# Optimization experiments

Measured on AMD Instinct MI355X. Metric: run time of the kernel, lower is better.

The kernel has to match this reference:

```python
import jax, jax.numpy as jnp
import numpy as np

KH, KW, STRIDE, PAD, DIL = 3, 3, 1, 1, 1


def setup_inputs() -> dict:
    key = jax.random.key(0)
    ks = jax.random.split(key, 4)
    B, C, H, W, O = 4, 256, 64, 64, 256
    K = KH * KW
    x = jax.random.normal(ks[0], (B, C, H, W), jnp.float32)
    # offset/mask conv params (original inits to zero; use small random so offsets are non-trivial)
    w_om = jax.random.normal(ks[1], (3 * K, C, KH, KW), jnp.float32) * 0.01
    b_om = jnp.zeros((3 * K,), jnp.float32)
    # main weight: kaiming_uniform_(a=1) -> gain = sqrt(2/(1+1^2)) = 1, bound = sqrt(3)/sqrt(fan_in)
    fan_in = C * K
    bound = float(np.sqrt(3.0) / np.sqrt(fan_in))
    weight = jax.random.uniform(ks[2], (O, C, KH, KW), jnp.float32, -bound, bound)
    bias = jnp.zeros((O,), jnp.float32)
    return {"x": x, "w_om": w_om, "b_om": b_om, "weight": weight, "bias": bias}


def _deform_conv2d(x, offset, mask, weight, bias):
    # torchvision.ops.deform_conv2d semantics, deformable_groups=1, stride=1, pad=1, dil=1
    B, C, H, W = x.shape
    K = KH * KW
    # torchvision offset layout: per-tap interleaved (y, x) pairs along channel dim
    off_y = offset[:, 0::2]  # [B, K, H, W]
    off_x = offset[:, 1::2]  # [B, K, H, W]
    ky = (jnp.repeat(jnp.arange(KH), KW) * DIL).astype(x.dtype)  # [K]
    kx = (jnp.tile(jnp.arange(KW), KH) * DIL).astype(x.dtype)    # [K]
    base_y = (jnp.arange(H) * STRIDE - PAD).astype(x.dtype)
    base_x = (jnp.arange(W) * STRIDE - PAD).astype(x.dtype)
    py = base_y[None, None, :, None] + ky[None, :, None, None] + off_y  # [B,K,H,W]
    px = base_x[None, None, None, :] + kx[None, :, None, None] + off_x  # [B,K,H,W]
    y0 = jnp.floor(py)
    x0 = jnp.floor(px)
    ly = py - y0
    lx = px - x0
    y0i = y0.astype(jnp.int32)
    x0i = x0.astype(jnp.int32)
    x_flat = x.reshape(B, C, H * W)

    def gather(yy, xx):
        # zero-padded gather of one bilinear corner -> [B, C, K, H, W]
        valid = ((yy >= 0) & (yy < H) & (xx >= 0) & (xx < W)).astype(x.dtype)
        idx = (jnp.clip(yy, 0, H - 1) * W + jnp.clip(xx, 0, W - 1)).reshape(B, -1)
        g = jax.vmap(lambda xf, i: jnp.take(xf, i, axis=1))(x_flat, idx)
        return g.reshape(B, C, K, H, W) * valid.reshape(B, 1, K, H, W)

    w00 = ((1 - ly) * (1 - lx))[:, None]
    w01 = ((1 - ly) * lx)[:, None]
    w10 = (ly * (1 - lx))[:, None]
    w11 = (ly * lx)[:, None]
    val = (gather(y0i, x0i) * w00 + gather(y0i, x0i + 1) * w01
           + gather(y0i + 1, x0i) * w10 + gather(y0i + 1, x0i + 1) * w11)
    cols = val * mask[:, None]  # modulated columns [B,C,K,H,W]
    out = jnp.einsum('bckhw,ock->bohw', cols, weight.reshape(weight.shape[0], C, K))
    return out + bias[None, :, None, None]


def reference(x, w_om, b_om, weight, bias):
    om = jax.lax.conv_general_dilated(
        x, w_om, (STRIDE, STRIDE), ((PAD, PAD), (PAD, PAD)),
        rhs_dilation=(DIL, DIL), dimension_numbers=('NCHW', 'OIHW', 'NCHW'),
    ) + b_om[None, :, None, None]
    K = KH * KW
    o1, o2, m = om[:, :K], om[:, K:2 * K], om[:, 2 * K:]
    offset = jnp.concatenate([o1, o2], axis=1)  # [B, 2K, H, W]
    mask = jax.nn.sigmoid(m)                    # [B, K, H, W]
    return _deform_conv2d(x, offset, mask, weight, bias)
```

## Files before the change

### kernel.cpp

```cpp
#include <hip/hip_runtime.h>
#include <stdint.h>

#define B_ 4
#define C_ 256
#define H_ 64
#define W_ 64
#define O_ 256
#define K_ 9
#define CK 2304
#define HW 4096
#define NTOT 16384

typedef __bf16 bf16x8 __attribute__((ext_vector_type(8)));
typedef __bf16 bf16x4 __attribute__((ext_vector_type(4)));
typedef float f32x4 __attribute__((ext_vector_type(4)));
typedef float f32x2 __attribute__((ext_vector_type(2)));
typedef f32x2 __attribute__((aligned(4))) f32x2u;

__device__ __forceinline__ uint16_t f2bf(float f) {
  uint32_t u = __builtin_bit_cast(uint32_t, f);
  return (uint16_t)((u + 0x7FFFu + ((u >> 16) & 1u)) >> 16);
}

__device__ __forceinline__ uint32_t pk_bf16(float a, float b) {
  uint16_t lo = __builtin_bit_cast(uint16_t, (__bf16)a);
  uint16_t hi = __builtin_bit_cast(uint16_t, (__bf16)b);
  return (uint32_t)lo | ((uint32_t)hi << 16);
}

__global__ void kA_prep(const float* __restrict__ weight, const float* __restrict__ w_om,
                        const float* __restrict__ x, uint16_t* __restrict__ wb,
                        uint16_t* __restrict__ womb, uint16_t* __restrict__ xT) {
  int bx = blockIdx.x;
  int t = threadIdx.x;
  if (bx < 256) {
    int o = bx, c = t;
    const float* wp = weight + (o * 256 + c) * 9;
#pragma unroll
    for (int k = 0; k < 9; ++k) wb[o * CK + k * 256 + c] = f2bf(wp[k]);
  } else if (bx < 283) {
    int j = bx - 256, c = t;
    const float* wp = w_om + (j * 256 + c) * 9;
#pragma unroll
    for (int k = 0; k < 9; ++k) womb[j * CK + k * 256 + c] = f2bf(wp[k]);
  } else if (bx < 288) {
    int j = 27 + (bx - 283), c = t;
#pragma unroll
    for (int k = 0; k < 9; ++k) womb[j * CK + k * 256 + c] = 0;
  } else {
    int bxl = bx - 288;
    int ct = bxl & 3;
    int hwt = (bxl >> 2) & 63;
    int b = bxl >> 8;
    int l = t & 63;
    int cq = t >> 6;

    __shared__ __align__(16) uint16_t tile[64 * 72];

    const float* xb = x + ((b * 256 + ct * 64) * HW) + hwt * 64;
#pragma unroll
    for (int i = 0; i < 16; ++i) {
      int c = cq * 16 + i;
      tile[l * 72 + c] = f2bf(xb[c * HW + l]);
    }
    __syncthreads();

    int hw = t >> 2;
    int c8 = (t & 3) * 8;
    uint16_t* dst = xT + ((size_t)b << 20) + (size_t)(hwt * 64 + hw) * 256 + ct * 64;
    *(uint4*)&dst[c8] = *(const uint4*)&tile[hw * 72 + c8];
    *(uint4*)&dst[c8 + 32] = *(const uint4*)&tile[hw * 72 + c8 + 32];
  }
}


struct GatherState {
  float wa0[4], wb0[4], wa1[4], wb1[4];
  bf16x4 r00[4], r01[4], r10[4], r11[4];
};

__device__ __forceinline__ void gather_issue(GatherState& S, const uint16_t* __restrict__ xb,
                                             const float* pypx_l,
                                             int kg, int rbase, int lane) {
#pragma unroll
  for (int j = 0; j < 4; ++j) {
    int nrow = rbase + j;
    float py = pypx_l[(0 * 9 + kg) * 64 + nrow];
    float px = pypx_l[(1 * 9 + kg) * 64 + nrow];
    float mk = pypx_l[(2 * 9 + kg) * 64 + nrow];
    float fy0 = floorf(py), fx0 = floorf(px);
    float ly = py - fy0, lx = px - fx0;
    int y0 = (int)fy0, x0 = (int)fx0;
    bool vy0 = ((unsigned)y0 < 64u), vy1 = ((unsigned)(y0 + 1) < 64u);
    bool vx0 = ((unsigned)x0 < 64u), vx1 = ((unsigned)(x0 + 1) < 64u);
    float w00 = (vy0 && vx0) ? (1.f - ly) * (1.f - lx) * mk : 0.f;
    float w01 = (vy0 && vx1) ? (1.f - ly) * lx * mk : 0.f;
    float w10 = (vy1 && vx0) ? ly * (1.f - lx) * mk : 0.f;
    float w11 = (vy1 && vx1) ? ly * lx * mk : 0.f;
    bool sel0 = (x0 >= 63);
    bool sel1 = (x0 >= 0);
    S.wa0[j] = (sel0 ? 0.f : w00) + (sel1 ? 0.f : w01);
    S.wb0[j] = (sel0 ? w00 : 0.f) + (sel1 ? w01 : 0.f);
    S.wa1[j] = (sel0 ? 0.f : w10) + (sel1 ? 0.f : w11);
    S.wb1[j] = (sel0 ? w10 : 0.f) + (sel1 ? w11 : 0.f);
    int bx0 = min(max(x0, 0), 62);
    int a0 = min(max(y0, 0), 63) * 64 + bx0;
    int a1 = min(max(y0 + 1, 0), 63) * 64 + bx0;
    S.r00[j] = *(const bf16x4*)&xb[a0 * 256 + lane * 4];
    S.r01[j] = *(const bf16x4*)&xb[a0 * 256 + 256 + lane * 4];
    S.r10[j] = *(const bf16x4*)&xb[a1 * 256 + lane * 4];
    S.r11[j] = *(const bf16x4*)&xb[a1 * 256 + 256 + lane * 4];
  }
}

__device__ __forceinline__ void gather_finish(const GatherState& S, uint16_t* bslab,
                                              int rbase, int lane) {
#pragma unroll
  for (int j = 0; j < 4; ++j) {
    int nrow = rbase + j;
    float v[4];
#pragma unroll
    for (int i = 0; i < 4; ++i)
      v[i] = S.wa0[j] * (float)S.r00[j][i] + S.wb0[j] * (float)S.r01[j][i] +
             S.wa1[j] * (float)S.r10[j][i] + S.wb1[j] * (float)S.r11[j][i];
    uint2 pk;
    pk.x = pk_bf16(v[0], v[1]);
    pk.y = pk_bf16(v[2], v[3]);
    int chunk = lane >> 1;
    int chs = (chunk & 24) | ((chunk & 7) ^ (nrow & 7));
    *(uint2*)&bslab[nrow * 256 + chs * 8 + (lane & 1) * 4] = pk;
  }
}

__device__ __forceinline__ void stageA(const uint16_t* __restrict__ wb, uint16_t* asbuf,
                                       int kbase, int t) {
#pragma unroll
  for (int i = 0; i < 4; ++i) {
    int rr = i * 64 + (t >> 3);
    const uint16_t* src = wb + rr * CK + kbase + (((t & 7) ^ (rr & 7)) << 3);
    __builtin_amdgcn_global_load_lds(
        (const __attribute__((address_space(1))) uint32_t*)src,
        (__attribute__((address_space(3))) uint32_t*)&asbuf[i * 4096 + t * 8], 16, 0, 0);
  }
}

__device__ __forceinline__ void mma_step(const uint16_t* AsP, const uint16_t* BsP,
                                         f32x4 acc[4][2], int wm, int wn, int lr, int q,
                                         int kt2) {
#pragma unroll
  for (int kc = 0; kc < 2; ++kc) {
    bf16x8 aF[4], bF[2];
#pragma unroll
    for (int i = 0; i < 4; ++i) {
      int row = wm * 64 + i * 16 + lr;
      aF[i] = *(const bf16x8*)&AsP[row * 64 + (((kc * 4 + q) ^ (row & 7)) << 3)];
    }
#pragma unroll
    for (int j = 0; j < 2; ++j) {
      int row = wn * 32 + j * 16 + lr;
      int kidx = kt2 * 8 + kc * 4 + q;
      int chs = (kidx & 24) | ((kidx & 7) ^ (row & 7));
      bF[j] = *(const bf16x8*)&BsP[row * 256 + chs * 8];
    }
#pragma unroll
    for (int i = 0; i < 4; ++i)
#pragma unroll
      for (int j = 0; j < 2; ++j)
        acc[i][j] = __builtin_amdgcn_mfma_f32_16x16x32_bf16(aF[i], bF[j], acc[i][j], 0, 0, 0);
  }
}

__global__ __launch_bounds__(512, 2) void k123(const uint16_t* __restrict__ wb,
                                               const uint16_t* __restrict__ womb,
                                               const uint16_t* __restrict__ xT,
                                               const float* __restrict__ b_om,
                                               const float* __restrict__ bias,
                                               float* __restrict__ out) {
  __shared__ __align__(16) uint16_t As[2][16384];
  __shared__ __align__(16) uint16_t Bs[16384];
  __shared__ float pypx_l[3 * 9 * 64];

  int t = threadIdx.x;
  int lane = t & 63;
  int wid = __builtin_amdgcn_readfirstlane(t >> 6);
  int lr = lane & 15, q = lane >> 4;
  int bx = blockIdx.x;
  int swz = (bx & 7) * 32 + (bx >> 3);
  int n0 = swz * 64;
  int b = n0 >> 12;
  int hw0 = n0 & 4095;
  const uint16_t* xb = xT + ((size_t)b << 20);

  {
    int ns4 = wid & 3;
    int kh2 = wid >> 2;
    int hw = (n0 + ns4 * 16 + lr) & 4095;
    int y = hw >> 6, xx = hw & 63;
    const uint16_t* zrow = womb + 31 * CK;

    f32x4 acc0 = {0.f, 0.f, 0.f, 0.f};
    f32x4 acc1 = {0.f, 0.f, 0.f, 0.f};

    int ks = kh2 ? 4 : 0;
    int ke = kh2 ? 9 : 4;
    for (int k = ks; k < ke; ++k) {
      int dy = k / 3, dx = k - dy * 3;
      int ny = y + dy - 1, nx = xx + dx - 1;
      bool valid = ((unsigned)ny < 64u) && ((unsigned)nx < 64u);
      int row = (min(max(ny, 0), 63) << 6) + min(max(nx, 0), 63);
      const uint16_t* bp = valid ? (xb + row * 256 + q * 8) : (zrow + q * 8);
      const uint16_t* ap = womb + lr * CK + k * 256 + q * 8;
#pragma unroll
      for (int kt = 0; kt < 8; ++kt) {
        int c0 = kt * 32;
        bf16x8 bF = *(const bf16x8*)&bp[c0];
        bf16x8 aF0 = *(const bf16x8*)&ap[c0];
        bf16x8 aF1 = *(const bf16x8*)&ap[16 * CK + c0];
        acc0 = __builtin_amdgcn_mfma_f32_16x16x32_bf16(aF0, bF, acc0, 0, 0, 0);
        acc1 = __builtin_amdgcn_mfma_f32_16x16x32_bf16(aF1, bF, acc1, 0, 0, 0);
      }
    }

    float* red = (float*)As;
    int base = ((kh2 * 4 + ns4) * 64 + lane) * 8;
#pragma unroll
    for (int r = 0; r < 4; ++r) {
      red[base + r] = acc0[r];
      red[base + 4 + r] = acc1[r];
    }
    __syncthreads();

    if (kh2 == 0) {
      int b0 = (ns4 * 64 + lane) * 8;
      int b1 = ((4 + ns4) * 64 + lane) * 8;
      int nn = ns4 * 16 + lr;
#pragma unroll
      for (int i = 0; i < 8; ++i) {
        float s = red[b0 + i] + red[b1 + i];
        int j = (i < 4) ? (q * 4 + i) : (16 + q * 4 + (i - 4));
        if (j < 27) {
          float v = s + b_om[j];
          if (j < 18) {
            int k = j >> 1;
            if ((j & 1) == 0)
              pypx_l[(0 * 9 + k) * 64 + nn] = (float)(y - 1 + k / 3) + v;
            else
              pypx_l[(1 * 9 + k) * 64 + nn] = (float)(xx - 1 + k % 3) + v;
          } else {
            pypx_l[(2 * 9 + (j - 18)) * 64 + nn] = 1.f / (1.f + __expf(-v));
          }
        }
      }
    }
    __syncthreads();
  }

  f32x4 acc[4][2];
  const f32x4 zero = {0.f, 0.f, 0.f, 0.f};
#pragma unroll
  for (int i = 0; i < 4; ++i)
#pragma unroll
    for (int j = 0; j < 2; ++j) acc[i][j] = zero;

  int wm = wid >> 1, wn = wid & 1;
  GatherState S;
  int wrow = wid * 8;

  gather_issue(S, xb, pypx_l, 0, wrow, lane);
  gather_finish(S, Bs, wrow, lane);
  gather_issue(S, xb, pypx_l, 0, wrow + 4, lane);
  gather_finish(S, Bs, wrow + 4, lane);
  stageA(wb, As[0], 0, t);
  __syncthreads();

  for (int k = 0; k < 9; ++k) {
    for (int kt2 = 0; kt2 < 4; ++kt2) {
      if (!(k == 8 && kt2 == 3)) {
        int kb2 = (kt2 == 3) ? (k + 1) * 256 : k * 256 + (kt2 + 1) * 64;
        stageA(wb, As[(kt2 + 1) & 1], kb2, t);
      }
      mma_step(As[kt2 & 1], Bs, acc, wm, wn, lr, q, kt2);
      __syncthreads();
    }
    if (k < 8) {
      gather_issue(S, xb, pypx_l, k + 1, wrow, lane);
      gather_finish(S, Bs, wrow, lane);
      gather_issue(S, xb, pypx_l, k + 1, wrow + 4, lane);
      gather_finish(S, Bs, wrow + 4, lane);
      __syncthreads();
    }
  }

#pragma unroll
  for (int i = 0; i < 4; ++i) {
#pragma unroll
    for (int r = 0; r < 4; ++r) {
      int o = wm * 64 + i * 16 + q * 4 + r;
      float bv = bias[o];
      float* orow = out + (b * O_ + o) * HW + hw0;
#pragma unroll
      for (int j = 0; j < 2; ++j) orow[wn * 32 + j * 16 + lr] = acc[i][j][r] + bv;
    }
  }
}

__global__ void k0_wconv(const float* __restrict__ weight, uint16_t* __restrict__ wb) {
  int idx = blockIdx.x * 256 + threadIdx.x;
  if (idx >= O_ * CK) return;
  int o = idx / CK;
  int rem = idx - o * CK;
  int k = rem >> 8;
  int c = rem & 255;
  wb[idx] = f2bf(weight[(o * C_ + c) * K_ + k]);
}

__global__ void k1_offconv(const float* __restrict__ x, const float* __restrict__ w_om,
                           const float* __restrict__ b_om, float* __restrict__ pypxmk) {
  int bx = blockIdx.x;
  int jq = bx % 7;
  int h = (bx / 7) % H_;
  int b = bx / (7 * H_);
  int t = threadIdx.x;
  int w = t & 63;
  int cs = __builtin_amdgcn_readfirstlane(t >> 6);

  float acc[4] = {0.f, 0.f, 0.f, 0.f};
  const float* xb = x + (b * C_) * HW;

  for (int ci = 0; ci < 64; ++ci) {
    int c = cs * 64 + ci;
    const float* xr = xb + c * HW;
    float xv[3][3];
#pragma unroll
    for (int r = 0; r < 3; ++r) {
      int y = h - 1 + r;
      bool yv = ((unsigned)y < 64u);
#pragma unroll
      for (int dx = 0; dx < 3; ++dx) {
        int xx = w - 1 + dx;
        bool v = yv && ((unsigned)xx < 64u);
        xv[r][dx] = v ? xr[y * 64 + xx] : 0.f;
      }
    }
    const float* wp = w_om + ((jq * 4) * C_ + c) * 9;
#pragma unroll
    for (int jj = 0; jj < 4; ++jj) {
      int j = jq * 4 + jj;
      int jeff = (j < 27) ? jj : 0;
      const float* wj = wp + jeff * (C_ * 9);
      float a = 0.f;
#pragma unroll
      for (int r = 0; r < 3; ++r)
#pragma unroll
        for (int dx = 0; dx < 3; ++dx)
          a = fmaf(xv[r][dx], wj[r * 3 + dx], a);
      acc[jj] += a;
    }
  }

  __shared__ float red[4][4][64];
#pragma unroll
  for (int jj = 0; jj < 4; ++jj) red[cs][jj][w] = acc[jj];
  __syncthreads();

  int jj = t >> 6;
  int j = jq * 4 + jj;
  if (j < 27) {
    float s = red[0][jj][w] + red[1][jj][w] + red[2][jj][w] + red[3][jj][w] + b_om[j];
    float* pyA = pypxmk;
    float* pxA = pypxmk + 147456;
    float* mkA = pypxmk + 294912;
    if (j < 18) {
      int k = j >> 1;
      int off = (b * 9 + k) * HW + h * 64 + w;
      if ((j & 1) == 0)
        pyA[off] = (float)(h - 1 + k / 3) + s;
      else
        pxA[off] = (float)(w - 1 + k % 3) + s;
    } else {
      int k = j - 18;
      mkA[(b * 9 + k) * HW + h * 64 + w] = 1.f / (1.f + __expf(-s));
    }
  }
}

__global__ void k2_fb(const float* __restrict__ x, const float* __restrict__ pypxmk,
                      uint16_t* __restrict__ cols) {
  int bx = blockIdx.x;
  int cg2 = bx & 15;
  int h = (bx >> 4) & 63;
  int b = bx >> 10;
  int t = threadIdx.x;
  int w = t & 63;
  int g = t >> 6;

  const float* pyA = pypxmk;
  const float* pxA = pypxmk + 147456;
  const float* mkA = pypxmk + 294912;

  __shared__ uint16_t tile[64 * 146];
  const float* xb = x + b * C_ * HW;
  int cbase = cg2 * 16 + g * 4;

#pragma unroll
  for (int k = 0; k < 9; ++k) {
    int poff = (b * 9 + k) * HW + h * 64 + w;
    float py = pyA[poff];
    float px = pxA[poff];
    float mk = mkA[poff];
    float fy0 = floorf(py), fx0 = floorf(px);
    float ly = py - fy0, lx = px - fx0;
    int y0 = (int)fy0, x0 = (int)fx0;
    bool vy0 = ((unsigned)y0 < 64u), vy1 = ((unsigned)(y0 + 1) < 64u);
    bool vx0 = ((unsigned)x0 < 64u), vx1 = ((unsigned)(x0 + 1) < 64u);
    float w00 = (vy0 && vx0) ? (1.f - ly) * (1.f - lx) * mk : 0.f;
    float w01 = (vy0 && vx1) ? (1.f - ly) * lx * mk : 0.f;
    float w10 = (vy1 && vx0) ? ly * (1.f - lx) * mk : 0.f;
    float w11 = (vy1 && vx1) ? ly * lx * mk : 0.f;
    bool sel0 = (x0 >= 63);
    bool sel1 = (x0 >= 0);
    float wa0 = (sel0 ? 0.f : w00) + (sel1 ? 0.f : w01);
    float wb0 = (sel0 ? w00 : 0.f) + (sel1 ? w01 : 0.f);
    float wa1 = (sel0 ? 0.f : w10) + (sel1 ? 0.f : w11);
    float wb1 = (sel0 ? w10 : 0.f) + (sel1 ? w11 : 0.f);
    int bx0 = min(max(x0, 0), 62);
    int a0 = min(max(y0, 0), 63) * 64 + bx0;
    int a1 = min(max(y0 + 1, 0), 63) * 64 + bx0;

#pragma unroll
    for (int cp = 0; cp < 2; ++cp) {
      const float* xcA = xb + (cbase + cp * 2) * HW;
      const float* xcB = xcA + HW;
      f32x2 A0 = *(const f32x2u*)&xcA[a0];
      f32x2 A1 = *(const f32x2u*)&xcA[a1];
      f32x2 B0 = *(const f32x2u*)&xcB[a0];
      f32x2 B1 = *(const f32x2u*)&xcB[a1];
      float rA = wa0 * A0.x + wb0 * A0.y + wa1 * A1.x + wb1 * A1.y;
      float rB = wa0 * B0.x + wb0 * B0.y + wa1 * B1.x + wb1 * B1.y;
      *(uint32_t*)&tile[w * 146 + k * 16 + g * 4 + cp * 2] = pk_bf16(rA, rB);
    }
  }
  __syncthreads();

#pragma unroll
  for (int it = 0; it < 18; ++it) {
    int u = t + it * 256;
    int wu = u / 72;
    int rem = u - wu * 72;
    int k = rem >> 3;
    int cd = rem & 7;
    uint32_t val = *(const uint32_t*)&tile[wu * 146 + rem * 2];
    int n = b * HW + h * 64 + wu;
    int dst = n * CK + k * 256 + cg2 * 16 + cd * 2;
    *(uint32_t*)&cols[dst] = val;
  }
}

__global__ void k3_flex(const uint16_t* __restrict__ wb, const uint16_t* __restrict__ cols,
                        const float* __restrict__ bias, float* __restrict__ out) {
  int bx = blockIdx.x;
  int mt = bx & 1;
  int nt = bx >> 1;
  int o0 = mt * 128;
  int n0 = nt * 128;
  int t = threadIdx.x;
  int lane = t & 63;
  int wid = t >> 6;
  int wm = wid >> 1, wn = wid & 1;
  int lr = lane & 15, q = lane >> 4;

  __shared__ __align__(16) uint16_t As[128 * 32];
  __shared__ __align__(16) uint16_t Bs[128 * 32];

  f32x4 acc[4][4];
  const f32x4 zero = {0.f, 0.f, 0.f, 0.f};
#pragma unroll
  for (int i = 0; i < 4; ++i)
#pragma unroll
    for (int j = 0; j < 4; ++j) acc[i][j] = zero;

  int r0 = t >> 2;
  int koff = (t & 3) * 8;
  const uint16_t* gA = wb + (o0 + r0) * CK + koff;
  const uint16_t* gB = cols + (n0 + r0) * CK + koff;

  for (int kt = 0; kt < 72; ++kt) {
    int k0 = kt * 32;
    __builtin_amdgcn_global_load_lds(
        (const __attribute__((address_space(1))) uint32_t*)(gA + k0),
        (__attribute__((address_space(3))) uint32_t*)&As[t * 8], 16, 0, 0);
    __builtin_amdgcn_global_load_lds(
        (const __attribute__((address_space(1))) uint32_t*)(gA + 64 * CK + k0),
        (__attribute__((address_space(3))) uint32_t*)&As[2048 + t * 8], 16, 0, 0);
    __builtin_amdgcn_global_load_lds(
        (const __attribute__((address_space(1))) uint32_t*)(gB + k0),
        (__attribute__((address_space(3))) uint32_t*)&Bs[t * 8], 16, 0, 0);
    __builtin_amdgcn_global_load_lds(
        (const __attribute__((address_space(1))) uint32_t*)(gB + 64 * CK + k0),
        (__attribute__((address_space(3))) uint32_t*)&Bs[2048 + t * 8], 16, 0, 0);
    __syncthreads();

    bf16x8 aF[4], bF[4];
#pragma unroll
    for (int i = 0; i < 4; ++i)
      aF[i] = *(const bf16x8*)&As[(wm * 64 + i * 16 + lr) * 32 + q * 8];
#pragma unroll
    for (int j = 0; j < 4; ++j)
      bF[j] = *(const bf16x8*)&Bs[(wn * 64 + j * 16 + lr) * 32 + q * 8];
#pragma unroll
    for (int i = 0; i < 4; ++i)
#pragma unroll
      for (int j = 0; j < 4; ++j)
        acc[i][j] = __builtin_amdgcn_mfma_f32_16x16x32_bf16(aF[i], bF[j], acc[i][j], 0, 0, 0);
    __syncthreads();
  }

  int bb = n0 >> 12;
  int hw0 = n0 & 4095;
#pragma unroll
  for (int i = 0; i < 4; ++i) {
#pragma unroll
    for (int r = 0; r < 4; ++r) {
      int o = o0 + wm * 64 + i * 16 + q * 4 + r;
      float bv = bias[o];
      float* orow = out + (bb * O_ + o) * HW + hw0;
#pragma unroll
      for (int j = 0; j < 4; ++j) orow[wn * 64 + j * 16 + lr] = acc[i][j][r] + bv;
    }
  }
}

extern "C" void kernel_launch(void* const* d_in, const int* in_sizes, int n_in,
                              void* d_out, int out_size, void* d_ws, size_t ws_size,
                              hipStream_t stream) {
  const float* x = (const float*)d_in[0];
  const float* w_om = (const float*)d_in[1];
  const float* b_om = (const float*)d_in[2];
  const float* weight = (const float*)d_in[3];
  const float* bias = (const float*)d_in[4];
  float* out = (float*)d_out;

  char* ws = (char*)d_ws;
  uint16_t* wb = (uint16_t*)ws;
  uint16_t* womb = (uint16_t*)(ws + 1179648);
  uint16_t* xT = (uint16_t*)(ws + 1327104);

  if (ws_size >= 11485184ull) {
    hipLaunchKernelGGL(kA_prep, dim3(1312), dim3(256), 0, stream, weight, w_om, x, wb, womb, xT);
    hipLaunchKernelGGL(k123, dim3(256), dim3(512), 0, stream, wb, womb, xT, b_om, bias, out);
  } else {
    float* pypx_fb = (float*)(ws + 1179648);
    uint16_t* colsf = (uint16_t*)(ws + 2949120);
    hipLaunchKernelGGL(k0_wconv, dim3(2304), dim3(256), 0, stream, weight, wb);
    hipLaunchKernelGGL(k1_offconv, dim3(4 * 64 * 7), dim3(256), 0, stream, x, w_om, b_om, pypx_fb);
    hipLaunchKernelGGL(k2_fb, dim3(4 * 64 * 16), dim3(256), 0, stream, x, pypx_fb, colsf);
    hipLaunchKernelGGL(k3_flex, dim3(256), dim3(256), 0, stream, wb, colsf, bias, out);
  }
}
```

Before: 158.7 us.

## Stage offset-conv prologue operands in LDS via async global_load_lds

```diff
diff --git a/kernel.cpp b/kernel.cpp
--- a/kernel.cpp
+++ b/kernel.cpp
@@ -192,63 +192,69 @@
   const uint16_t* xb = xT + ((size_t)b << 20);
 
   {
-    int ns4 = wid & 3;
-    int kh2 = wid >> 2;
-    int hw = (n0 + ns4 * 16 + lr) & 4095;
-    int y = hw >> 6, xx = hw & 63;
+    uint16_t* Apro = As[0];
+    int jh = wid >> 2, ng = wid & 3;
     const uint16_t* zrow = womb + 31 * CK;
-
-    f32x4 acc0 = {0.f, 0.f, 0.f, 0.f};
-    f32x4 acc1 = {0.f, 0.f, 0.f, 0.f};
-
-    int ks = kh2 ? 4 : 0;
-    int ke = kh2 ? 9 : 4;
-    for (int k = ks; k < ke; ++k) {
-      int dy = k / 3, dx = k - dy * 3;
-      int ny = y + dy - 1, nx = xx + dx - 1;
-      bool valid = ((unsigned)ny < 64u) && ((unsigned)nx < 64u);
-      int row = (min(max(ny, 0), 63) << 6) + min(max(nx, 0), 63);
-      const uint16_t* bp = valid ? (xb + row * 256 + q * 8) : (zrow + q * 8);
-      const uint16_t* ap = womb + lr * CK + k * 256 + q * 8;
+    f32x4 accp = {0.f, 0.f, 0.f, 0.f};
+
+    for (int k = 0; k < 9; ++k) {
+      int dy = k / 3 - 1, dx = k - (k / 3) * 3 - 1;
+#pragma unroll
+      for (int i = 0; i < 2; ++i) {
+        int id = i * 512 + t;
+        int row = id >> 5, c5 = id & 31;
+        int cs = (c5 & 24) | ((c5 & 7) ^ (row & 7));
+        const uint16_t* src = womb + row * CK + k * 256 + cs * 8;
+        __builtin_amdgcn_global_load_lds(
+            (const __attribute__((address_space(1))) uint32_t*)src,
+            (__attribute__((address_space(3))) uint32_t*)&Apro[row * 256 + c5 * 8], 16, 0, 0);
+      }
+#pragma unroll
+      for (int i = 0; i < 4; ++i) {
+        int id = i * 512 + t;
+        int nrow = id >> 5, c5 = id & 31;
+        int hw = (n0 + nrow) & 4095;
+        int y = hw >> 6, xx = hw & 63;
+        int ny = y + dy, nx = xx + dx;
+        bool valid = ((unsigned)ny < 64u) && ((unsigned)nx < 64u);
+        int row_g = (ny << 6) + nx;
+        int cs = (c5 & 24) | ((c5 & 7) ^ (nrow & 7));
+        const uint16_t* src = valid ? (xb + row_g * 256 + cs * 8) : (zrow + cs * 8);
+        __builtin_amdgcn_global_load_lds(
+            (const __attribute__((address_space(1))) uint32_t*)src,
+            (__attribute__((address_space(3))) uint32_t*)&Bs[nrow * 256 + c5 * 8], 16, 0, 0);
+      }
+      __syncthreads();
 #pragma unroll
       for (int kt = 0; kt < 8; ++kt) {
-        int c0 = kt * 32;
-        bf16x8 bF = *(const bf16x8*)&bp[c0];
-        bf16x8 aF0 = *(const bf16x8*)&ap[c0];
-        bf16x8 aF1 = *(const bf16x8*)&ap[16 * CK + c0];
-        acc0 = __builtin_amdgcn_mfma_f32_16x16x32_bf16(aF0, bF, acc0, 0, 0, 0);
-        acc1 = __builtin_amdgcn_mfma_f32_16x16x32_bf16(aF1, bF, acc1, 0, 0, 0);
+        int kidx = kt * 4 + q;
+        int arow = jh * 16 + lr;
+        int achs = (kidx & 24) | ((kidx & 7) ^ (arow & 7));
+        bf16x8 aF = *(const bf16x8*)&Apro[arow * 256 + achs * 8];
+        int brow = ng * 16 + lr;
+        int bchs = (kidx & 24) | ((kidx & 7) ^ (brow & 7));
+        bf16x8 bF = *(const bf16x8*)&Bs[brow * 256 + bchs * 8];
+        accp = __builtin_amdgcn_mfma_f32_16x16x32_bf16(aF, bF, accp, 0, 0, 0);
       }
-    }
-
-    float* red = (float*)As;
-    int base = ((kh2 * 4 + ns4) * 64 + lane) * 8;
+      __syncthreads();
+    }
+
+    int nn = ng * 16 + lr;
+    int hwp = (n0 + nn) & 4095;
+    int yp = hwp >> 6, xp = hwp & 63;
 #pragma unroll
     for (int r = 0; r < 4; ++r) {
-      red[base + r] = acc0[r];
-      red[base + 4 + r] = acc1[r];
-    }
-    __syncthreads();
-
-    if (kh2 == 0) {
-      int b0 = (ns4 * 64 + lane) * 8;
-      int b1 = ((4 + ns4) * 64 + lane) * 8;
-      int nn = ns4 * 16 + lr;
-#pragma unroll
-      for (int i = 0; i < 8; ++i) {
-        float s = red[b0 + i] + red[b1 + i];
-        int j = (i < 4) ? (q * 4 + i) : (16 + q * 4 + (i - 4));
-        if (j < 27) {
-          float v = s + b_om[j];
-          if (j < 18) {
-            int k = j >> 1;
-            if ((j & 1) == 0)
-              pypx_l[(0 * 9 + k) * 64 + nn] = (float)(y - 1 + k / 3) + v;
-            else
-              pypx_l[(1 * 9 + k) * 64 + nn] = (float)(xx - 1 + k % 3) + v;
-          } else {
-            pypx_l[(2 * 9 + (j - 18)) * 64 + nn] = 1.f / (1.f + __expf(-v));
-          }
+      int j = jh * 16 + q * 4 + r;
+      if (j < 27) {
+        float v = accp[r] + b_om[j];
+        if (j < 18) {
+          int k = j >> 1;
+          if ((j & 1) == 0)
+            pypx_l[(0 * 9 + k) * 64 + nn] = (float)(yp - 1 + k / 3) + v;
+          else
+            pypx_l[(1 * 9 + k) * 64 + nn] = (float)(xp - 1 + k % 3) + v;
+        } else {
+          pypx_l[(2 * 9 + (j - 18)) * 64 + nn] = 1.f / (1.f + __expf(-v));
         }
       }
     }
```

Result: faster. 147.3 us (-7.1%).
